# Performance work log

Hardware: AMD Instinct MI355X
Metric: run time of the kernel (lower is better)

The kernel has to match this reference:

```python
import jax, jax.numpy as jnp
import numpy as np

# pywt coif5 dec_lo (30 taps)
COIF5_DEC_LO = np.array([
    -9.517657273819165e-08, -1.6744288576823017e-07, 2.0637618513646814e-06,
    3.7346551751414047e-06, -2.1315026809955787e-05, -4.134043227251251e-05,
    0.00014054114970203437, 0.00030225958181306315, -0.0006381313430451114,
    -0.0016628637020130838, 0.0024333732126576722, 0.006764185448053083,
    -0.009164231162481846, -0.01976177894257264, 0.03268357426711183,
    0.0412892087501817, -0.10557420870333893, -0.06203596396290357,
    0.4379916261718371, 0.7742896036529562, 0.4215662066908515,
    -0.05204316317624377, -0.09192001055969624, 0.02816802897093635,
    0.023408156785839195, -0.010131117519849788, -0.004159358781386048,
    0.0021782363581090178, 0.00035858968789573785, -0.00021208083980379827,
], dtype=np.float32)


def _hilbert(x):
    # scipy.fftpack.hilbert: y_j = 1j*sign(j)*X_j, DC and Nyquist zeroed
    n = x.size
    X = np.fft.fft(x)
    sign = np.zeros(n)
    sign[1:(n + 1) // 2] = 1.0
    sign[n // 2 + 1:] = -1.0
    return np.real(np.fft.ifft(X * 1j * sign)).astype(np.float32)


def _make_filters():
    gl = COIF5_DEC_LO
    L = gl.size
    # QMF: dec_hi[k] = (-1)^(k+1) * dec_lo[L-1-k]
    gh = (((-1.0) ** (np.arange(L) + 1)) * gl[::-1]).astype(np.float32)
    fl = _hilbert(gl)
    fh = _hilbert(gh)
    return (jnp.asarray(gl), jnp.asarray(gh), jnp.asarray(fl), jnp.asarray(fh))


# torch bicubic (a=-0.75), scale 0.5, align_corners=False: src = 2*i + 0.5,
# fractional offset is always 0.5 -> fixed 4-tap stride-2 stencil.
_W0, _W1, _W2, _W3 = -0.09375, 0.59375, 0.59375, -0.09375


def _down2_last(x):
    # downsample last axis by 2 with edge-clamped borders (matches torch clamp)
    n = x.shape[-1]
    pad = [(0, 0)] * (x.ndim - 1) + [(1, 1)]
    xp = jnp.pad(x, pad, mode='edge')
    base = 2 * jnp.arange(n // 2)  # tap positions in padded coords
    return (_W0 * xp[..., base] + _W1 * xp[..., base + 1]
            + _W2 * xp[..., base + 2] + _W3 * xp[..., base + 3])


def _downsample(x):
    x = _down2_last(x)                                        # W axis
    x = jnp.swapaxes(_down2_last(jnp.swapaxes(x, -1, -2)), -1, -2)  # H axis
    return x


def _qwt(image, gl, gh, fl, fh):
    # In the source, _column/_row_convolve never shift X per tap and the
    # centered crop exactly removes the reflect padding, so
    # colfilter(X, h) == rowfilter(X, h) == X * sum(h)  (exact).
    filt = lambda x, h: x * jnp.sum(h)

    gl_d = _downsample(filt(image, gl))
    gh_d = _downsample(filt(image, gh))
    fl_d = _downsample(filt(image, fl))
    fh_d = _downsample(filt(image, fh))

    lglg = filt(gl_d, gl); lghg = filt(gl_d, gh); lglf = filt(gl_d, fl); lghf = filt(gl_d, fh)
    hglg = filt(gh_d, gl); hghg = filt(gh_d, gh); hglf = filt(gh_d, fl); hghf = filt(gh_d, fh)
    lflg = filt(fl_d, gl); lfhg = filt(fl_d, gh); lflf = filt(fl_d, fl); lfhf = filt(fl_d, fh)
    hflg = filt(fh_d, gl); hfhg = filt(fh_d, gh); hflf = filt(fh_d, fl); hfhf = filt(fh_d, fh)

    return (jnp.concatenate((lglg, lflg, lglf, lflf), axis=1),
            jnp.concatenate((lghg, lfhg, lghf, lfhf), axis=1),
            jnp.concatenate((hglg, hflg, hglf, hflf), axis=1),
            jnp.concatenate((hghg, hfhg, hghf, hfhf), axis=1))


def setup_inputs() -> dict:
    key = jax.random.key(0)
    image = jax.random.normal(key, (16, 3, 512, 512), dtype=jnp.float32)
    gl, gh, fl, fh = _make_filters()
    return {"image": image, "gl": gl, "gh": gh, "fl": fl, "fh": fh}


def reference(image, gl, gh, fl, fh):
    return _qwt(image, gl, gh, fl, fh)
```

## Files before the change

kernel.cpp:

```cpp
#include <hip/hip_runtime.h>


#define BW0 -0.09375f
#define BW1  0.59375f
#define BW2  0.59375f
#define BW3 -0.09375f

#define H_IN  512
#define W_IN  512
#define H_OUT 256
#define W_OUT 256
#define PLANE_OUT (H_OUT * W_OUT)
#define TENSOR_STRIDE (16 * 12 * PLANE_OUT)

typedef __attribute__((ext_vector_type(4))) float f32x4;

__global__ __launch_bounds__(256) void qwt_fused_kernel(
    const float* __restrict__ img,
    const float* __restrict__ gl, const float* __restrict__ gh,
    const float* __restrict__ fl, const float* __restrict__ fh,
    float* __restrict__ out)
{
    __shared__ float s_scale[16];

    const int tid = threadIdx.x;

    if (tid < 64) {
        float vgl = 0.f, vgh = 0.f, vfl = 0.f, vfh = 0.f;
        if (tid < 30) { vgl = gl[tid]; vgh = gh[tid]; vfl = fl[tid]; vfh = fh[tid]; }
        #pragma unroll
        for (int m = 32; m >= 1; m >>= 1) {
            vgl += __shfl_xor(vgl, m);
            vgh += __shfl_xor(vgh, m);
            vfl += __shfl_xor(vfl, m);
            vfh += __shfl_xor(vfh, m);
        }
        if (tid < 16) {
            const int t = tid >> 2, cb = tid & 3;
            const float A = (t < 2) ? ((cb & 1) ? vfl : vgl)
                                    : ((cb & 1) ? vfh : vgh);
            const float B = (t & 1) ? ((cb < 2) ? vgh : vfh)
                                    : ((cb < 2) ? vgl : vfl);
            s_scale[tid] = A * B;
        }
    }
    __syncthreads();

    float sc[16];
    #pragma unroll
    for (int i = 0; i < 16; ++i) sc[i] = s_scale[i];

    const int idx = blockIdx.x * 256 + tid;
    const int w4 = idx & 63;
    const int hp = (idx >> 6) & 127;
    const int bc = idx >> 13;
    const int c  = bc % 3;
    const int b  = bc / 3;

    const float* plane = img + (size_t)bc * (H_IN * W_IN);

    int r[6];
    #pragma unroll
    for (int i = 0; i < 6; ++i) {
        int rr = 4 * hp - 1 + i;
        r[i] = rr < 0 ? 0 : (rr > H_IN - 1 ? H_IN - 1 : rr);
    }

    const int cbase = w4 * 8;
    int clo = cbase - 1; if (clo < 0) clo = 0;
    int chi = cbase + 8; if (chi > W_IN - 1) chi = W_IN - 1;

    float hv[6][4];
    #pragma unroll
    for (int i = 0; i < 6; ++i) {
        const float* rowp = plane + (size_t)r[i] * W_IN;
        const float4 a  = *(const float4*)(rowp + cbase);
        const float4 b4 = *(const float4*)(rowp + cbase + 4);
        const float v0 = rowp[clo];
        const float v9 = rowp[chi];
        const float v1 = a.x,  v2 = a.y,  v3 = a.z,  v4 = a.w;
        const float v5 = b4.x, v6 = b4.y, v7 = b4.z, v8 = b4.w;
        hv[i][0] = BW0 * v0 + BW1 * v1 + BW2 * v2 + BW3 * v3;
        hv[i][1] = BW0 * v2 + BW1 * v3 + BW2 * v4 + BW3 * v5;
        hv[i][2] = BW0 * v4 + BW1 * v5 + BW2 * v6 + BW3 * v7;
        hv[i][3] = BW0 * v6 + BW1 * v7 + BW2 * v8 + BW3 * v9;
    }

    float d0[4], d1[4];
    #pragma unroll
    for (int j = 0; j < 4; ++j) {
        d0[j] = BW0 * hv[0][j] + BW1 * hv[1][j] + BW2 * hv[2][j] + BW3 * hv[3][j];
        d1[j] = BW0 * hv[2][j] + BW1 * hv[3][j] + BW2 * hv[4][j] + BW3 * hv[5][j];
    }

    const size_t obase = (size_t)b * (12 * PLANE_OUT)
                       + (size_t)c * PLANE_OUT
                       + (size_t)(2 * hp) * W_OUT
                       + (size_t)(w4 * 4);
    #pragma unroll
    for (int t = 0; t < 4; ++t) {
        #pragma unroll
        for (int cb = 0; cb < 4; ++cb) {
            const float s = sc[t * 4 + cb];
            float* p0 = out + (size_t)t * TENSOR_STRIDE
                            + obase
                            + (size_t)cb * (3 * PLANE_OUT);
            float* p1 = p0 + W_OUT;
            f32x4 o0, o1;
            o0.x = d0[0] * s; o0.y = d0[1] * s; o0.z = d0[2] * s; o0.w = d0[3] * s;
            o1.x = d1[0] * s; o1.y = d1[1] * s; o1.z = d1[2] * s; o1.w = d1[3] * s;
            __builtin_nontemporal_store(o0, (f32x4*)p0);
            __builtin_nontemporal_store(o1, (f32x4*)p1);
        }
    }
}

extern "C" void kernel_launch(void* const* d_in, const int* in_sizes, int n_in,
                              void* d_out, int out_size, void* d_ws, size_t ws_size,
                              hipStream_t stream) {
    const float* img = (const float*)d_in[0];
    const float* gl  = (const float*)d_in[1];
    const float* gh  = (const float*)d_in[2];
    const float* fl  = (const float*)d_in[3];
    const float* fh  = (const float*)d_in[4];
    float* out = (float*)d_out;

    const int threads = 256;
    const int blocks  = (16 * 3 * 256 * 256 / 8) / threads;
    qwt_fused_kernel<<<blocks, threads, 0, stream>>>(img, gl, gh, fl, fh, out);
}
```

Measured before the change: 245.7 us.

## Stage downsampled tile in LDS and emit contiguous per-wave output slabs

Each block now covers a 16-row by 256-column slab of one plane. Each thread computes two row-pairs and writes them to shared memory. After a barrier, each wave owns one of the four output tensors and streams 16 contiguous rows for each of its four sub-bands, so the stores are long contiguous runs instead of scattered 16-byte writes across sixteen destinations. The grid shrinks from 1536 to 768 blocks with more work per thread. This adds 16 KB of LDS per block and a barrier, and the reduced block count could lower occupancy and latency hiding.

```diff
diff --git a/kernel.cpp b/kernel.cpp
--- a/kernel.cpp
+++ b/kernel.cpp
@@ -22,6 +22,7 @@
     float* __restrict__ out)
 {
     __shared__ float s_scale[16];
+    __shared__ __align__(16) float sD[16][W_OUT];
 
     const int tid = threadIdx.x;
 
@@ -44,73 +45,84 @@
             s_scale[tid] = A * B;
         }
     }
-    __syncthreads();
 
-    float sc[16];
-    #pragma unroll
-    for (int i = 0; i < 16; ++i) sc[i] = s_scale[i];
-
-    const int idx = blockIdx.x * 256 + tid;
-    const int w4 = idx & 63;
-    const int hp = (idx >> 6) & 127;
-    const int bc = idx >> 13;
-    const int c  = bc % 3;
-    const int b  = bc / 3;
+    const int blk = blockIdx.x;
+    const int s   = blk & 15;
+    const int bc  = blk >> 4;
 
     const float* plane = img + (size_t)bc * (H_IN * W_IN);
 
-    int r[6];
-    #pragma unroll
-    for (int i = 0; i < 6; ++i) {
-        int rr = 4 * hp - 1 + i;
-        r[i] = rr < 0 ? 0 : (rr > H_IN - 1 ? H_IN - 1 : rr);
-    }
+    const int w4  = tid & 63;
+    const int hpL = tid >> 6;
 
     const int cbase = w4 * 8;
     int clo = cbase - 1; if (clo < 0) clo = 0;
     int chi = cbase + 8; if (chi > W_IN - 1) chi = W_IN - 1;
 
-    float hv[6][4];
     #pragma unroll
-    for (int i = 0; i < 6; ++i) {
-        const float* rowp = plane + (size_t)r[i] * W_IN;
-        const float4 a  = *(const float4*)(rowp + cbase);
-        const float4 b4 = *(const float4*)(rowp + cbase + 4);
-        const float v0 = rowp[clo];
-        const float v9 = rowp[chi];
-        const float v1 = a.x,  v2 = a.y,  v3 = a.z,  v4 = a.w;
-        const float v5 = b4.x, v6 = b4.y, v7 = b4.z, v8 = b4.w;
-        hv[i][0] = BW0 * v0 + BW1 * v1 + BW2 * v2 + BW3 * v3;
-        hv[i][1] = BW0 * v2 + BW1 * v3 + BW2 * v4 + BW3 * v5;
-        hv[i][2] = BW0 * v4 + BW1 * v5 + BW2 * v6 + BW3 * v7;
-        hv[i][3] = BW0 * v6 + BW1 * v7 + BW2 * v8 + BW3 * v9;
+    for (int u = 0; u < 2; ++u) {
+        const int hp = hpL + 4 * u;
+
+        int r[6];
+        #pragma unroll
+        for (int i = 0; i < 6; ++i) {
+            int rr = 32 * s + 4 * hp - 1 + i;
+            r[i] = rr < 0 ? 0 : (rr > H_IN - 1 ? H_IN - 1 : rr);
+        }
+
+        float hv[6][4];
+        #pragma unroll
+        for (int i = 0; i < 6; ++i) {
+            const float* rowp = plane + (size_t)r[i] * W_IN;
+            const float4 a  = *(const float4*)(rowp + cbase);
+            const float4 b4 = *(const float4*)(rowp + cbase + 4);
+            const float v0 = rowp[clo];
+            const float v9 = rowp[chi];
+            const float v1 = a.x,  v2 = a.y,  v3 = a.z,  v4 = a.w;
+            const float v5 = b4.x, v6 = b4.y, v7 = b4.z, v8 = b4.w;
+            hv[i][0] = BW0 * v0 + BW1 * v1 + BW2 * v2 + BW3 * v3;
+            hv[i][1] = BW0 * v2 + BW1 * v3 + BW2 * v4 + BW3 * v5;
+            hv[i][2] = BW0 * v4 + BW1 * v5 + BW2 * v6 + BW3 * v7;
+            hv[i][3] = BW0 * v6 + BW1 * v7 + BW2 * v8 + BW3 * v9;
+        }
+
+        f32x4 d0, d1;
+        d0.x = BW0 * hv[0][0] + BW1 * hv[1][0] + BW2 * hv[2][0] + BW3 * hv[3][0];
+        d0.y = BW0 * hv[0][1] + BW1 * hv[1][1] + BW2 * hv[2][1] + BW3 * hv[3][1];
+        d0.z = BW0 * hv[0][2] + BW1 * hv[1][2] + BW2 * hv[2][2] + BW3 * hv[3][2];
+        d0.w = BW0 * hv[0][3] + BW1 * hv[1][3] + BW2 * hv[2][3] + BW3 * hv[3][3];
+        d1.x = BW0 * hv[2][0] + BW1 * hv[3][0] + BW2 * hv[4][0] + BW3 * hv[5][0];
+        d1.y = BW0 * hv[2][1] + BW1 * hv[3][1] + BW2 * hv[4][1] + BW3 * hv[5][1];
+        d1.z = BW0 * hv[2][2] + BW1 * hv[3][2] + BW2 * hv[4][2] + BW3 * hv[5][2];
+        d1.w = BW0 * hv[2][3] + BW1 * hv[3][3] + BW2 * hv[4][3] + BW3 * hv[5][3];
+
+        *(f32x4*)&sD[2 * hp    ][4 * w4] = d0;
+        *(f32x4*)&sD[2 * hp + 1][4 * w4] = d1;
     }
 
-    float d0[4], d1[4];
+    __syncthreads();
+
+    const int wave = tid >> 6;
+    const int lane = tid & 63;
+    const int c  = bc % 3;
+    const int b  = bc / 3;
+
+    float* outT = out + (size_t)wave * TENSOR_STRIDE
+                + (size_t)b * (12 * PLANE_OUT)
+                + (size_t)c * PLANE_OUT
+                + (size_t)(16 * s) * W_OUT
+                + (size_t)(4 * lane);
+
     #pragma unroll
-    for (int j = 0; j < 4; ++j) {
-        d0[j] = BW0 * hv[0][j] + BW1 * hv[1][j] + BW2 * hv[2][j] + BW3 * hv[3][j];
-        d1[j] = BW0 * hv[2][j] + BW1 * hv[3][j] + BW2 * hv[4][j] + BW3 * hv[5][j];
-    }
-
-    const size_t obase = (size_t)b * (12 * PLANE_OUT)
-                       + (size_t)c * PLANE_OUT
-                       + (size_t)(2 * hp) * W_OUT
-                       + (size_t)(w4 * 4);
-    #pragma unroll
-    for (int t = 0; t < 4; ++t) {
+    for (int cb = 0; cb < 4; ++cb) {
+        const float sc = s_scale[wave * 4 + cb];
+        float* p = outT + (size_t)cb * (3 * PLANE_OUT);
         #pragma unroll
-        for (int cb = 0; cb < 4; ++cb) {
-            const float s = sc[t * 4 + cb];
-            float* p0 = out + (size_t)t * TENSOR_STRIDE
-                            + obase
-                            + (size_t)cb * (3 * PLANE_OUT);
-            float* p1 = p0 + W_OUT;
-            f32x4 o0, o1;
-            o0.x = d0[0] * s; o0.y = d0[1] * s; o0.z = d0[2] * s; o0.w = d0[3] * s;
-            o1.x = d1[0] * s; o1.y = d1[1] * s; o1.z = d1[2] * s; o1.w = d1[3] * s;
-            __builtin_nontemporal_store(o0, (f32x4*)p0);
-            __builtin_nontemporal_store(o1, (f32x4*)p1);
+        for (int rr = 0; rr < 16; ++rr) {
+            f32x4 v = *(const f32x4*)&sD[rr][4 * lane];
+            f32x4 o;
+            o.x = v.x * sc; o.y = v.y * sc; o.z = v.z * sc; o.w = v.w * sc;
+            __builtin_nontemporal_store(o, (f32x4*)(p + (size_t)rr * W_OUT));
         }
     }
 }
@@ -126,6 +138,6 @@
     float* out = (float*)d_out;
 
     const int threads = 256;
-    const int blocks  = (16 * 3 * 256 * 256 / 8) / threads;
+    const int blocks  = 48 * 16;
     qwt_fused_kernel<<<blocks, threads, 0, stream>>>(img, gl, gh, fl, fh, out);
 }
```

Measured after the change: 246.4 us. Within noise of the previous version (+0.3%).
